# Kernel tuning notes

Measured on AMD Instinct MI355X. Metric: run time of the kernel, lower is better.

## Reference

```python
import jax, jax.numpy as jnp
import numpy as np

SOS, EOS = 0, 1
MAXLEN = 128
EPS = 1e-5


def setup_inputs() -> dict:
    key = jax.random.key(0)
    ks = jax.random.split(key, 10)
    B, T, Hc, Hs, V, Hm = 64, 1024, 512, 512, 64, 128
    h = jax.random.normal(ks[0], (B, T, Hc), dtype=jnp.float32)
    x_seq_lens = jax.random.randint(ks[1], (B,), 1, T + 1).astype(jnp.int32)
    s = 0.05
    return {
        "h": h,
        "W_ih": jax.random.normal(ks[2], (4 * Hs, V + Hc), dtype=jnp.float32) * s,
        "W_hh": jax.random.normal(ks[3], (4 * Hs, Hs), dtype=jnp.float32) * s,
        "b_ih": jax.random.normal(ks[4], (4 * Hs,), dtype=jnp.float32) * s,
        "b_hh": jax.random.normal(ks[5], (4 * Hs,), dtype=jnp.float32) * s,
        "fc1_w": jax.random.normal(ks[6], (Hm, Hs + Hc), dtype=jnp.float32) * s,
        "fc1_b": jax.random.normal(ks[7], (Hm,), dtype=jnp.float32) * s,
        "fc2_w": jax.random.normal(ks[8], (V, Hm), dtype=jnp.float32) * s,
        "x_seq_lens": x_seq_lens,
    }


def reference(h, W_ih, W_hh, b_ih, b_hh, fc1_w, fc1_b, fc2_w, x_seq_lens):
    B, T, Hc = h.shape
    Hs = W_hh.shape[1]
    V = fc2_w.shape[0]
    # attention length mask [B, T]
    mask = (jnp.arange(T)[None, :] < x_seq_lens[:, None]).astype(h.dtype)
    sos = jax.nn.one_hot(jnp.full((B,), SOS), V, dtype=h.dtype)
    x0 = jnp.concatenate([sos, h[:, 0, :]], axis=-1)  # [B, V+Hc]
    carry0 = (x0, jnp.zeros((B, Hs), h.dtype), jnp.zeros((B, Hs), h.dtype),
              jnp.full((B,), MAXLEN, jnp.int32))

    def step(carry, t):
        x, hs, cs, lens = carry
        # single-layer LSTM cell, torch gate order i,f,g,o
        gates = x @ W_ih.T + hs @ W_hh.T + b_ih + b_hh
        i, f, g, o = jnp.split(gates, 4, axis=-1)
        cs = jax.nn.sigmoid(f) * cs + jax.nn.sigmoid(i) * jnp.tanh(g)
        hs = jax.nn.sigmoid(o) * jnp.tanh(cs)
        # dot-product attention (apply_proj=False, num_heads=1)
        e = jnp.einsum('bd,btd->bt', hs, h)
        exps = jnp.exp(e - jnp.max(e)) * mask  # MaskedSoftmax: global-max shift
        a = exps / (exps.sum(-1, keepdims=True) + EPS)
        ctx = jnp.einsum('bt,btd->bd', a, h)
        # chardist: two stacked linears (no nonlinearity), then softmax
        feat = jnp.concatenate([hs, ctx], axis=-1)
        logits = (feat @ fc1_w.T + fc1_b) @ fc2_w.T
        y_hat = jax.nn.softmax(logits, axis=-1)
        hit = (jnp.argmax(y_hat, axis=-1) == EOS) & (lens > t)
        lens = jnp.where(hit, t + 1, lens)
        x = jnp.concatenate([y_hat, ctx], axis=-1)  # decode mode (y=None)
        return (x, hs, cs, lens), (y_hat, a)

    (_, _, _, lens), (y_hats, atts) = jax.lax.scan(step, carry0, jnp.arange(MAXLEN))
    y_hats = jnp.transpose(y_hats, (1, 0, 2))              # [B, L, V]
    attentions = jnp.transpose(atts, (1, 0, 2))[:, None]   # [B, 1, L, T]
    return y_hats, lens, attentions
```

## Files before the change

kernel.cpp:

```cpp
#include <hip/hip_runtime.h>
#include <math.h>

typedef unsigned short ushort_t;
typedef unsigned int uint_t;

#define OFF_XT    0
#define OFF_CS    102400
#define OFF_E     135168
#define OFF_MD    200704
#define OFF_LENS  204800
#define OFF_W2    204864
#define OFF_B2    270400
#define OFF_CP    270464
#define OFF_HB16F 1319040
#define WS_NEED   ((size_t)(1319040 + 16777216) * 4)

#define OUT_YH   0
#define OUT_LENS 524288
#define OUT_ATT  524352

__device__ __forceinline__ float sigf(float x) { return 1.0f / (1.0f + __expf(-x)); }
__device__ __forceinline__ float dot4(float4 a, float4 b) {
    return a.x * b.x + a.y * b.y + a.z * b.z + a.w * b.w;
}
__device__ __forceinline__ uint_t bf16rne(float x) {
    uint_t u = __float_as_uint(x);
    return (u + 0x7FFFu + ((u >> 16) & 1u)) >> 16;
}
#define BLO(u) __uint_as_float((u) << 16)
#define BHI(u) __uint_as_float((u) & 0xFFFF0000u)

__global__ void k_init(const float* __restrict__ h, float* __restrict__ ws) {
    int blk = blockIdx.x, tid = threadIdx.x;
    int idx = blk * 256 + tid;
    if (idx < 102400) {
        int k = idx >> 6, b = idx & 63;
        float v = 0.0f;
        if (k == 0) v = 1.0f;
        else if (k >= 64 && k < 576) v = h[(size_t)b * 524288 + (k - 64)];
        ws[OFF_XT + idx] = v;
    }
    if (blk >= 400 && blk < 528)
        ws[OFF_CS + (blk - 400) * 256 + tid] = 0.0f;
    if (blk == 527 && tid < 64) ((int*)ws)[OFF_LENS + tid] = 128;
}

__global__ void k_hconv(const float* __restrict__ h, float* __restrict__ ws) {
    size_t i = ((size_t)blockIdx.x * 256 + threadIdx.x) * 8;
    float4 a = *(const float4*)(h + i);
    float4 b = *(const float4*)(h + i + 4);
    uint4 o;
    o.x = bf16rne(a.x) | (bf16rne(a.y) << 16);
    o.y = bf16rne(a.z) | (bf16rne(a.w) << 16);
    o.z = bf16rne(b.x) | (bf16rne(b.y) << 16);
    o.w = bf16rne(b.z) | (bf16rne(b.w) << 16);
    *(uint4*)((ushort_t*)(ws + OFF_HB16F) + i) = o;
}

__global__ void k_fuse(const float* __restrict__ fc1w, const float* __restrict__ fc1b,
                       const float* __restrict__ fc2w, float* __restrict__ ws) {
    int blk = blockIdx.x;
    int v = blk >> 2, kc = blk & 3;
    int k = kc * 256 + threadIdx.x;
    float acc = 0.0f;
#pragma unroll 8
    for (int m = 0; m < 128; m++) acc += fc2w[v * 128 + m] * fc1w[(size_t)m * 1024 + k];
    ws[OFF_W2 + (size_t)v * 1024 + k] = acc;
    if (kc == 0 && threadIdx.x == 0) {
        float bb = 0.0f;
        for (int m = 0; m < 128; m++) bb += fc2w[v * 128 + m] * fc1b[m];
        ws[OFF_B2 + v] = bb;
    }
}

__global__ __launch_bounds__(1024) void k_gates(
        const float* __restrict__ Wih, const float* __restrict__ Whh,
        const float* __restrict__ bih, const float* __restrict__ bhh,
        float* __restrict__ ws, int p) {
    const int tid = threadIdx.x;
    const int lane = tid & 63;
    const int w = tid >> 6;
    const int hs_in  = 576 + (p ? 512 : 0);
    const int hs_out = 576 + (p ? 0 : 512);
    __shared__ float gpart[8192];
    const int u0 = blockIdx.x * 2;
    const int wq = __builtin_amdgcn_readfirstlane(w);
    float acc[2][4] = {{0, 0, 0, 0}, {0, 0, 0, 0}};
    int k0 = wq * 68, k1 = k0 + 68;
    int kx1 = k1 < 576 ? k1 : 576;
#pragma unroll 2
    for (int k = k0; k < kx1; k += 4) {
        float4 xv;
        xv.x = ws[OFF_XT + (k + 0) * 64 + lane];
        xv.y = ws[OFF_XT + (k + 1) * 64 + lane];
        xv.z = ws[OFF_XT + (k + 2) * 64 + lane];
        xv.w = ws[OFF_XT + (k + 3) * 64 + lane];
#pragma unroll
        for (int uu = 0; uu < 2; ++uu)
#pragma unroll
            for (int g = 0; g < 4; ++g)
                acc[uu][g] += dot4(*(const float4*)&Wih[(size_t)(g * 512 + u0 + uu) * 576 + k], xv);
    }
    int kh0 = k0 > 576 ? k0 : 576;
#pragma unroll 2
    for (int k = kh0; k < k1; k += 4) {
        float4 xv;
        xv.x = ws[OFF_XT + (hs_in + (k - 576) + 0) * 64 + lane];
        xv.y = ws[OFF_XT + (hs_in + (k - 576) + 1) * 64 + lane];
        xv.z = ws[OFF_XT + (hs_in + (k - 576) + 2) * 64 + lane];
        xv.w = ws[OFF_XT + (hs_in + (k - 576) + 3) * 64 + lane];
#pragma unroll
        for (int uu = 0; uu < 2; ++uu)
#pragma unroll
            for (int g = 0; g < 4; ++g)
                acc[uu][g] += dot4(*(const float4*)&Whh[(size_t)(g * 512 + u0 + uu) * 512 + (k - 576)], xv);
    }
#pragma unroll
    for (int uu = 0; uu < 2; ++uu)
#pragma unroll
        for (int g = 0; g < 4; ++g)
            gpart[((w * 2 + uu) * 4 + g) * 64 + lane] = acc[uu][g];
    __syncthreads();
    if (tid < 128) {
        int uu = tid >> 6, b = tid & 63;
        int u = u0 + uu;
        float g4[4];
#pragma unroll
        for (int g = 0; g < 4; ++g) {
            float s = 0.0f;
#pragma unroll
            for (int ww = 0; ww < 16; ++ww) s += gpart[((ww * 2 + uu) * 4 + g) * 64 + b];
            g4[g] = s + bih[g * 512 + u] + bhh[g * 512 + u];
        }
        int idx = u * 64 + b;
        float co = ws[OFF_CS + idx];
        float I = sigf(g4[0]), F = sigf(g4[1]), G = tanhf(g4[2]), O = sigf(g4[3]);
        float cn = F * co + I * G;
        ws[OFF_CS + idx] = cn;
        ws[OFF_XT + (size_t)(hs_out + u) * 64 + b] = O * tanhf(cn);
    }
}

__global__ __launch_bounds__(256) void k_attn16(const int* __restrict__ slen,
                                                float* __restrict__ ws, int p) {
    const int blk = blockIdx.x;
    const int tid = threadIdx.x;
    const int lane = tid & 63;
    const int w = __builtin_amdgcn_readfirstlane(tid >> 6);
    const int rg = lane >> 4, cl = lane & 15;
    const int hs_out = 576 + (p ? 0 : 512);
    const int b = blk >> 5, sb = blk & 31;
    const int L = slen[b];
    const int t0 = sb * 32;
    __shared__ float hs_sh[512];
    __shared__ float e_part[128];
    __shared__ float e_sh[32];
    __shared__ float wt_sh[32];
    const ushort_t* hb = (const ushort_t*)(ws + OFF_HB16F)
                       + ((size_t)b * 1024 + t0) * 512 + w * 128 + cl * 8;
    uint4 r0 = *(const uint4*)(hb + (size_t)(rg * 8 + 0) * 512);
    uint4 r1 = *(const uint4*)(hb + (size_t)(rg * 8 + 1) * 512);
    uint4 r2 = *(const uint4*)(hb + (size_t)(rg * 8 + 2) * 512);
    uint4 r3 = *(const uint4*)(hb + (size_t)(rg * 8 + 3) * 512);
    uint4 r4 = *(const uint4*)(hb + (size_t)(rg * 8 + 4) * 512);
    uint4 r5 = *(const uint4*)(hb + (size_t)(rg * 8 + 5) * 512);
    uint4 r6 = *(const uint4*)(hb + (size_t)(rg * 8 + 6) * 512);
    uint4 r7 = *(const uint4*)(hb + (size_t)(rg * 8 + 7) * 512);
    hs_sh[tid]       = ws[OFF_XT + (size_t)(hs_out + tid) * 64 + b];
    hs_sh[256 + tid] = ws[OFF_XT + (size_t)(hs_out + 256 + tid) * 64 + b];
    __syncthreads();
    float hsv[8];
#pragma unroll
    for (int j = 0; j < 8; ++j) hsv[j] = hs_sh[w * 128 + cl * 8 + j];
#define EROW(J, R)                                                                  \
    {                                                                               \
        float part = BLO(R.x) * hsv[0] + BHI(R.x) * hsv[1]                          \
                   + BLO(R.y) * hsv[2] + BHI(R.y) * hsv[3]                          \
                   + BLO(R.z) * hsv[4] + BHI(R.z) * hsv[5]                          \
                   + BLO(R.w) * hsv[6] + BHI(R.w) * hsv[7];                         \
        part += __shfl_xor(part, 1);                                                \
        part += __shfl_xor(part, 2);                                                \
        part += __shfl_xor(part, 4);                                                \
        part += __shfl_xor(part, 8);                                                \
        if (cl == 0) e_part[w * 32 + rg * 8 + (J)] = part;                          \
    }
    EROW(0, r0) EROW(1, r1) EROW(2, r2) EROW(3, r3)
    EROW(4, r4) EROW(5, r5) EROW(6, r6) EROW(7, r7)
#undef EROW
    __syncthreads();
    if (tid < 32) {
        float e = e_part[tid] + e_part[32 + tid] + e_part[64 + tid] + e_part[96 + tid];
        e_sh[tid] = e;
        ws[OFF_E + (size_t)b * 1024 + t0 + tid] = e;
    }
    __syncthreads();
    if (tid < 32) {
        float m = e_sh[0];
#pragma unroll
        for (int j = 1; j < 32; ++j) m = fmaxf(m, e_sh[j]);
        int tg = t0 + tid;
        wt_sh[tid] = (tg < L) ? __expf(e_sh[tid] - m) : 0.0f;
        if (tid == 0) ws[OFF_MD + (b * 32 + sb) * 2] = m;
    }
    __syncthreads();
    float acc[8] = {0, 0, 0, 0, 0, 0, 0, 0};
#define PVROW(J, R)                                                                 \
    {                                                                               \
        float wt = wt_sh[rg * 8 + (J)];                                             \
        acc[0] += wt * BLO(R.x); acc[1] += wt * BHI(R.x);                           \
        acc[2] += wt * BLO(R.y); acc[3] += wt * BHI(R.y);                           \
        acc[4] += wt * BLO(R.z); acc[5] += wt * BHI(R.z);                           \
        acc[6] += wt * BLO(R.w); acc[7] += wt * BHI(R.w);                           \
    }
    PVROW(0, r0) PVROW(1, r1) PVROW(2, r2) PVROW(3, r3)
    PVROW(4, r4) PVROW(5, r5) PVROW(6, r6) PVROW(7, r7)
#undef PVROW
#pragma unroll
    for (int k = 0; k < 8; ++k) {
        acc[k] += __shfl_xor(acc[k], 16);
        acc[k] += __shfl_xor(acc[k], 32);
    }
    if (rg == 0) {
        float4 o0; o0.x = acc[0]; o0.y = acc[1]; o0.z = acc[2]; o0.w = acc[3];
        float4 o1; o1.x = acc[4]; o1.y = acc[5]; o1.z = acc[6]; o1.w = acc[7];
        float* cp = ws + OFF_CP + (size_t)(b * 32 + sb) * 512 + w * 128 + cl * 8;
        *(float4*)cp = o0;
        *(float4*)(cp + 4) = o1;
    }
    if (tid == 0) {
        float D = 0.0f;
#pragma unroll
        for (int tl = 0; tl < 32; ++tl) D += wt_sh[tl];
        ws[OFF_MD + (b * 32 + sb) * 2 + 1] = D;
    }
}

__global__ void k_attn(const float* __restrict__ h, const int* __restrict__ slen,
                       float* __restrict__ ws, int p) {
    const int blk = blockIdx.x;
    const int tid = threadIdx.x;
    const int lane = tid & 63;
    const int w = tid >> 6;
    const int hs_out = 576 + (p ? 0 : 512);
    const int b = blk >> 4, sb = blk & 15;
    const int L = slen[b];
    const int t0 = sb * 64;
    __shared__ float stage[4096];
    __shared__ float hs_sh[512];
    __shared__ float e_sh[8];
    const float* hb = h + ((size_t)b * 1024 + t0) * 512;
    hs_sh[tid]       = ws[OFF_XT + (size_t)(hs_out + tid) * 64 + b];
    hs_sh[256 + tid] = ws[OFF_XT + (size_t)(hs_out + 256 + tid) * 64 + b];
    __syncthreads();
    float hsv[8];
#pragma unroll
    for (int j = 0; j < 8; ++j) hsv[j] = hs_sh[lane * 8 + j];
    float m_run = -INFINITY, D = 0.0f, accx = 0.0f, accy = 0.0f;
    for (int c = 0; c < 8; ++c) {
        const float* gsrc = hb + (size_t)c * 4096 + tid * 4;
        float4 tv0 = *(const float4*)(gsrc);
        float4 tv1 = *(const float4*)(gsrc + 1024);
        float4 tv2 = *(const float4*)(gsrc + 2048);
        float4 tv3 = *(const float4*)(gsrc + 3072);
        __syncthreads();
        *(float4*)&stage[tid * 4]        = tv0;
        *(float4*)&stage[1024 + tid * 4] = tv1;
        *(float4*)&stage[2048 + tid * 4] = tv2;
        *(float4*)&stage[3072 + tid * 4] = tv3;
        __syncthreads();
#pragma unroll
        for (int rr = 0; rr < 2; ++rr) {
            int tl = w * 2 + rr;
            const float4* rp = (const float4*)&stage[tl * 512 + lane * 8];
            float4 pp = rp[0], qq = rp[1];
            float part = pp.x * hsv[0] + pp.y * hsv[1] + pp.z * hsv[2] + pp.w * hsv[3]
                       + qq.x * hsv[4] + qq.y * hsv[5] + qq.z * hsv[6] + qq.w * hsv[7];
#pragma unroll
            for (int mm = 1; mm < 64; mm <<= 1) part += __shfl_xor(part, mm);
            if (lane == 0) {
                e_sh[tl] = part;
                ws[OFF_E + (size_t)b * 1024 + t0 + c * 8 + tl] = part;
            }
        }
        __syncthreads();
        float cm = e_sh[0];
#pragma unroll
        for (int j = 1; j < 8; ++j) cm = fmaxf(cm, e_sh[j]);
        float m_new = fmaxf(m_run, cm);
        float sc = __expf(m_run - m_new);
        accx *= sc; accy *= sc; D *= sc;
        m_run = m_new;
#pragma unroll
        for (int tl = 0; tl < 8; ++tl) {
            int tg = t0 + c * 8 + tl;
            float wt = (tg < L) ? __expf(e_sh[tl] - m_run) : 0.0f;
            D += wt;
            float2 hv = *(const float2*)&stage[tl * 512 + tid * 2];
            accx += wt * hv.x;
            accy += wt * hv.y;
        }
    }
    float2 o2; o2.x = accx; o2.y = accy;
    *(float2*)&ws[OFF_CP + (size_t)(b * 16 + sb) * 512 + tid * 2] = o2;
    if (tid == 0) {
        ws[OFF_MD + (b * 16 + sb) * 2]     = m_run;
        ws[OFF_MD + (b * 16 + sb) * 2 + 1] = D;
    }
}

__global__ void k_comb(const int* __restrict__ slen, float* __restrict__ ws,
                       float* __restrict__ out, int p, int ts, int ns) {
    const int b = blockIdx.x, tid = threadIdx.x;
    const int hs_out = 576 + (p ? 0 : 512);
    __shared__ float red[256];
    __shared__ float feat[1024];
    __shared__ float sc_sh[32];
    __shared__ float lg_s[64];
    const int nent = 64 * ns;
    float mx = -INFINITY;
    for (int i = tid; i < nent; i += 256) mx = fmaxf(mx, ws[OFF_MD + i * 2]);
    red[tid] = mx;
    __syncthreads();
    for (int s = 128; s > 0; s >>= 1) {
        if (tid < s) red[tid] = fmaxf(red[tid], red[tid + s]);
        __syncthreads();
    }
    float m_g = red[0];
    __syncthreads();
    if (tid < ns) {
        float mi = ws[OFF_MD + (b * ns + tid) * 2];
        float Di = ws[OFF_MD + (b * ns + tid) * 2 + 1];
        float s = __expf(mi - m_g);
        sc_sh[tid] = s;
        red[tid] = s * Di;
    }
    __syncthreads();
    float dn = 0.0f;
    for (int j = 0; j < ns; ++j) dn += red[j];
    float inv = 1.0f / (dn + 1e-5f);
    float cx = 0.0f, cy = 0.0f;
    for (int i = 0; i < ns; ++i) {
        float s = sc_sh[i];
        float2 v = *(const float2*)&ws[OFF_CP + (size_t)(b * ns + i) * 512 + tid * 2];
        cx += s * v.x;
        cy += s * v.y;
    }
    cx *= inv; cy *= inv;
    feat[512 + tid * 2] = cx;
    feat[512 + tid * 2 + 1] = cy;
    ws[OFF_XT + (size_t)(64 + tid * 2) * 64 + b] = cx;
    ws[OFF_XT + (size_t)(64 + tid * 2 + 1) * 64 + b] = cy;
    feat[tid * 2]     = ws[OFF_XT + (size_t)(hs_out + tid * 2) * 64 + b];
    feat[tid * 2 + 1] = ws[OFF_XT + (size_t)(hs_out + tid * 2 + 1) * 64 + b];
    int L = slen[b];
#pragma unroll
    for (int q = 0; q < 4; ++q) {
        int t = tid + 256 * q;
        float e = ws[OFF_E + (size_t)b * 1024 + t];
        float a = (t < L) ? __expf(e - m_g) * inv : 0.0f;
        out[OUT_ATT + (size_t)b * 131072 + (size_t)ts * 1024 + t] = a;
    }
    __syncthreads();
    int v = tid >> 2, qq = tid & 3;
    const float4* w4 = (const float4*)(ws + OFF_W2 + (size_t)v * 1024 + qq * 256);
    const float4* f4 = (const float4*)feat + qq * 64;
    float acc = 0.0f;
#pragma unroll 8
    for (int k = 0; k < 64; ++k) acc += dot4(w4[k], f4[k]);
    acc += __shfl_xor(acc, 1);
    acc += __shfl_xor(acc, 2);
    if (qq == 0) lg_s[v] = acc;
    __syncthreads();
    if (tid < 64) {
        float lg = lg_s[tid] + ws[OFF_B2 + tid];
        float mxv = lg;
#pragma unroll
        for (int mm = 1; mm < 64; mm <<= 1) mxv = fmaxf(mxv, __shfl_xor(mxv, mm));
        float ev = __expf(lg - mxv);
        float s = ev;
#pragma unroll
        for (int mm = 1; mm < 64; mm <<= 1) s += __shfl_xor(s, mm);
        float y = ev / s;
        out[OUT_YH + (size_t)b * 8192 + ts * 64 + tid] = y;
        ws[OFF_XT + (size_t)tid * 64 + b] = y;
        float av = lg;
        int ai = tid;
#pragma unroll
        for (int mm = 1; mm < 64; mm <<= 1) {
            float ov = __shfl_xor(av, mm);
            int oi = __shfl_xor(ai, mm);
            if (ov > av || (ov == av && oi < ai)) { av = ov; ai = oi; }
        }
        if (tid == 0) {
            int* lens = (int*)ws + OFF_LENS;
            if (ai == 1 && lens[b] > ts) lens[b] = ts + 1;
            if (ts == 127) out[OUT_LENS + b] = (float)lens[b];
        }
    }
}

extern "C" void kernel_launch(void* const* d_in, const int* in_sizes, int n_in,
                              void* d_out, int out_size, void* d_ws, size_t ws_size,
                              hipStream_t stream) {
    (void)in_sizes; (void)n_in; (void)out_size;
    const float* h    = (const float*)d_in[0];
    const float* Wih  = (const float*)d_in[1];
    const float* Whh  = (const float*)d_in[2];
    const float* bih  = (const float*)d_in[3];
    const float* bhh  = (const float*)d_in[4];
    const float* fc1w = (const float*)d_in[5];
    const float* fc1b = (const float*)d_in[6];
    const float* fc2w = (const float*)d_in[7];
    const int*   slen = (const int*)d_in[8];
    float* ws  = (float*)d_ws;
    float* out = (float*)d_out;
    const bool use16 = (ws_size >= WS_NEED);

    k_init<<<528, 256, 0, stream>>>(h, ws);
    k_fuse<<<256, 256, 0, stream>>>(fc1w, fc1b, fc2w, ws);
    if (use16) k_hconv<<<16384, 256, 0, stream>>>(h, ws);
    for (int t = 0; t < 128; t++) {
        int p = t & 1;
        k_gates<<<256, 1024, 0, stream>>>(Wih, Whh, bih, bhh, ws, p);
        if (use16) {
            k_attn16<<<2048, 256, 0, stream>>>(slen, ws, p);
            k_comb<<<64, 256, 0, stream>>>(slen, ws, out, p, t, 32);
        } else {
            k_attn<<<1024, 256, 0, stream>>>(h, slen, ws, p);
            k_comb<<<64, 256, 0, stream>>>(slen, ws, out, p, t, 16);
        }
    }
}
```

Before: 6.112 ms.

## Split LSTM gates into x/hh parts and overlap hh-matmul with attention

Splits the gate computation so the input-projection part (W_ih times x) runs in its own kernel, while the recurrent W_hh times hs product for the next step is computed by extra blocks inside the attention kernel. Both read the same fresh hidden state, so the recurrent matmul is taken off the serial per-step chain. Attention blocks also skip the context accumulation for chunks beyond the sequence length. The combine kernel is rewritten with 512 threads to handle 1024-wide features directly. The price is a more complex dependency chain through the GHH workspace buffer and mixed block roles within one launch.

```diff
diff --git a/kernel.cpp b/kernel.cpp
--- a/kernel.cpp
+++ b/kernel.cpp
@@ -12,8 +12,9 @@
 #define OFF_W2    204864
 #define OFF_B2    270400
 #define OFF_CP    270464
-#define OFF_HB16F 1319040
-#define WS_NEED   ((size_t)(1319040 + 16777216) * 4)
+#define OFF_GHH   1319040
+#define OFF_HB16F 1450112
+#define WS_NEED   ((size_t)(1450112 + 16777216) * 4)
 
 #define OUT_YH   0
 #define OUT_LENS 524288
@@ -58,7 +59,8 @@
 }
 
 __global__ void k_fuse(const float* __restrict__ fc1w, const float* __restrict__ fc1b,
-                       const float* __restrict__ fc2w, float* __restrict__ ws) {
+                       const float* __restrict__ fc2w, const float* __restrict__ bih,
+                       const float* __restrict__ bhh, float* __restrict__ ws) {
     int blk = blockIdx.x;
     int v = blk >> 2, kc = blk & 3;
     int k = kc * 256 + threadIdx.x;
@@ -70,6 +72,293 @@
         float bb = 0.0f;
         for (int m = 0; m < 128; m++) bb += fc2w[v * 128 + m] * fc1b[m];
         ws[OFF_B2 + v] = bb;
+    }
+#pragma unroll
+    for (int rep = 0; rep < 2; ++rep) {
+        int idx = (blk * 256 + threadIdx.x) * 2 + rep;
+        int r = idx >> 6;
+        ws[OFF_GHH + idx] = bih[r] + bhh[r];
+    }
+}
+
+__global__ __launch_bounds__(512) void k_gatesx(const float* __restrict__ Wih,
+                                                float* __restrict__ ws) {
+    const int tid = threadIdx.x;
+    const int lane = tid & 63;
+    const int w = tid >> 6;
+    __shared__ float gpart[4096];
+    const int u0 = blockIdx.x * 2;
+    const int wq = __builtin_amdgcn_readfirstlane(w);
+    float acc[2][4] = {{0, 0, 0, 0}, {0, 0, 0, 0}};
+    int k0 = wq * 72, k1 = k0 + 72;
+#pragma unroll 2
+    for (int k = k0; k < k1; k += 4) {
+        float4 xv;
+        xv.x = ws[OFF_XT + (k + 0) * 64 + lane];
+        xv.y = ws[OFF_XT + (k + 1) * 64 + lane];
+        xv.z = ws[OFF_XT + (k + 2) * 64 + lane];
+        xv.w = ws[OFF_XT + (k + 3) * 64 + lane];
+#pragma unroll
+        for (int uu = 0; uu < 2; ++uu)
+#pragma unroll
+            for (int g = 0; g < 4; ++g)
+                acc[uu][g] += dot4(*(const float4*)&Wih[(size_t)(g * 512 + u0 + uu) * 576 + k], xv);
+    }
+#pragma unroll
+    for (int uu = 0; uu < 2; ++uu)
+#pragma unroll
+        for (int g = 0; g < 4; ++g)
+            gpart[((w * 2 + uu) * 4 + g) * 64 + lane] = acc[uu][g];
+    __syncthreads();
+    if (tid < 128) {
+        int uu = tid >> 6, b = tid & 63;
+        int u = u0 + uu;
+        float g4[4];
+#pragma unroll
+        for (int g = 0; g < 4; ++g) {
+            float s = ws[OFF_GHH + (size_t)(g * 512 + u) * 64 + b];
+#pragma unroll
+            for (int ww = 0; ww < 8; ++ww) s += gpart[((ww * 2 + uu) * 4 + g) * 64 + b];
+            g4[g] = s;
+        }
+        int idx = u * 64 + b;
+        float co = ws[OFF_CS + idx];
+        float I = sigf(g4[0]), F = sigf(g4[1]), G = tanhf(g4[2]), O = sigf(g4[3]);
+        float cn = F * co + I * G;
+        ws[OFF_CS + idx] = cn;
+        ws[OFF_XT + (size_t)(576 + u) * 64 + b] = O * tanhf(cn);
+    }
+}
+
+__global__ __launch_bounds__(256) void k_hh_attn(const int* __restrict__ slen,
+                                                 const float* __restrict__ Whh,
+                                                 const float* __restrict__ bih,
+                                                 const float* __restrict__ bhh,
+                                                 float* __restrict__ ws) {
+    const int blk = blockIdx.x;
+    const int tid = threadIdx.x;
+    const int lane = tid & 63;
+    __shared__ float smem[2048];
+    if (blk < 256) {
+        const int w = tid >> 6;
+        const int u0 = blk * 2;
+        const int wq = __builtin_amdgcn_readfirstlane(w);
+        float acc[2][4] = {{0, 0, 0, 0}, {0, 0, 0, 0}};
+        int k0 = wq * 128, k1 = k0 + 128;
+#pragma unroll 2
+        for (int k = k0; k < k1; k += 4) {
+            float4 xv;
+            xv.x = ws[OFF_XT + (576 + k + 0) * 64 + lane];
+            xv.y = ws[OFF_XT + (576 + k + 1) * 64 + lane];
+            xv.z = ws[OFF_XT + (576 + k + 2) * 64 + lane];
+            xv.w = ws[OFF_XT + (576 + k + 3) * 64 + lane];
+#pragma unroll
+            for (int uu = 0; uu < 2; ++uu)
+#pragma unroll
+                for (int g = 0; g < 4; ++g)
+                    acc[uu][g] += dot4(*(const float4*)&Whh[(size_t)(g * 512 + u0 + uu) * 512 + k], xv);
+        }
+#pragma unroll
+        for (int uu = 0; uu < 2; ++uu)
+#pragma unroll
+            for (int g = 0; g < 4; ++g)
+                smem[((w * 2 + uu) * 4 + g) * 64 + lane] = acc[uu][g];
+        __syncthreads();
+        if (tid < 128) {
+            int uu = tid >> 6, b = tid & 63;
+            int u = u0 + uu;
+#pragma unroll
+            for (int g = 0; g < 4; ++g) {
+                int r = g * 512 + u;
+                float s = bih[r] + bhh[r];
+#pragma unroll
+                for (int ww = 0; ww < 4; ++ww) s += smem[((ww * 2 + uu) * 4 + g) * 64 + b];
+                ws[OFF_GHH + (size_t)r * 64 + b] = s;
+            }
+        }
+        return;
+    }
+    float* hs_sh  = smem;
+    float* e_part = smem + 512;
+    float* e_sh   = smem + 640;
+    float* wt_sh  = smem + 672;
+    const int ab = blk - 256;
+    const int w = __builtin_amdgcn_readfirstlane(tid >> 6);
+    const int rg = lane >> 4, cl = lane & 15;
+    const int b = ab >> 5, sb = ab & 31;
+    const int L = slen[b];
+    const int t0 = sb * 32;
+    const ushort_t* hb = (const ushort_t*)(ws + OFF_HB16F)
+                       + ((size_t)b * 1024 + t0) * 512 + w * 128 + cl * 8;
+    uint4 r0 = *(const uint4*)(hb + (size_t)(rg * 8 + 0) * 512);
+    uint4 r1 = *(const uint4*)(hb + (size_t)(rg * 8 + 1) * 512);
+    uint4 r2 = *(const uint4*)(hb + (size_t)(rg * 8 + 2) * 512);
+    uint4 r3 = *(const uint4*)(hb + (size_t)(rg * 8 + 3) * 512);
+    uint4 r4 = *(const uint4*)(hb + (size_t)(rg * 8 + 4) * 512);
+    uint4 r5 = *(const uint4*)(hb + (size_t)(rg * 8 + 5) * 512);
+    uint4 r6 = *(const uint4*)(hb + (size_t)(rg * 8 + 6) * 512);
+    uint4 r7 = *(const uint4*)(hb + (size_t)(rg * 8 + 7) * 512);
+    hs_sh[tid]       = ws[OFF_XT + (size_t)(576 + tid) * 64 + b];
+    hs_sh[256 + tid] = ws[OFF_XT + (size_t)(576 + 256 + tid) * 64 + b];
+    __syncthreads();
+    float hsv[8];
+#pragma unroll
+    for (int j = 0; j < 8; ++j) hsv[j] = hs_sh[w * 128 + cl * 8 + j];
+#define EROW(J, R)                                                                  \
+    {                                                                               \
+        float part = BLO(R.x) * hsv[0] + BHI(R.x) * hsv[1]                          \
+                   + BLO(R.y) * hsv[2] + BHI(R.y) * hsv[3]                          \
+                   + BLO(R.z) * hsv[4] + BHI(R.z) * hsv[5]                          \
+                   + BLO(R.w) * hsv[6] + BHI(R.w) * hsv[7];                         \
+        part += __shfl_xor(part, 1);                                                \
+        part += __shfl_xor(part, 2);                                                \
+        part += __shfl_xor(part, 4);                                                \
+        part += __shfl_xor(part, 8);                                                \
+        if (cl == 0) e_part[w * 32 + rg * 8 + (J)] = part;                          \
+    }
+    EROW(0, r0) EROW(1, r1) EROW(2, r2) EROW(3, r3)
+    EROW(4, r4) EROW(5, r5) EROW(6, r6) EROW(7, r7)
+#undef EROW
+    __syncthreads();
+    if (tid < 32) {
+        float e = e_part[tid] + e_part[32 + tid] + e_part[64 + tid] + e_part[96 + tid];
+        e_sh[tid] = e;
+        ws[OFF_E + (size_t)b * 1024 + t0 + tid] = e;
+    }
+    __syncthreads();
+    if (tid < 32) {
+        float m = e_sh[0];
+#pragma unroll
+        for (int j = 1; j < 32; ++j) m = fmaxf(m, e_sh[j]);
+        int tg = t0 + tid;
+        wt_sh[tid] = (tg < L) ? __expf(e_sh[tid] - m) : 0.0f;
+        if (tid == 0) ws[OFF_MD + (b * 32 + sb) * 2] = m;
+    }
+    __syncthreads();
+    int nr = L - t0;
+    nr = nr < 0 ? 0 : (nr > 32 ? 32 : nr);
+    if (nr > 0) {
+        float acc[8] = {0, 0, 0, 0, 0, 0, 0, 0};
+#define PVROW(J, R)                                                                 \
+        {                                                                           \
+            float wt = wt_sh[rg * 8 + (J)];                                         \
+            acc[0] += wt * BLO(R.x); acc[1] += wt * BHI(R.x);                       \
+            acc[2] += wt * BLO(R.y); acc[3] += wt * BHI(R.y);                       \
+            acc[4] += wt * BLO(R.z); acc[5] += wt * BHI(R.z);                       \
+            acc[6] += wt * BLO(R.w); acc[7] += wt * BHI(R.w);                       \
+        }
+        PVROW(0, r0) PVROW(1, r1) PVROW(2, r2) PVROW(3, r3)
+        PVROW(4, r4) PVROW(5, r5) PVROW(6, r6) PVROW(7, r7)
+#undef PVROW
+#pragma unroll
+        for (int k = 0; k < 8; ++k) {
+            acc[k] += __shfl_xor(acc[k], 16);
+            acc[k] += __shfl_xor(acc[k], 32);
+        }
+        if (rg == 0) {
+            float4 o0; o0.x = acc[0]; o0.y = acc[1]; o0.z = acc[2]; o0.w = acc[3];
+            float4 o1; o1.x = acc[4]; o1.y = acc[5]; o1.z = acc[6]; o1.w = acc[7];
+            float* cp = ws + OFF_CP + (size_t)(b * 32 + sb) * 512 + w * 128 + cl * 8;
+            *(float4*)cp = o0;
+            *(float4*)(cp + 4) = o1;
+        }
+    }
+    if (tid == 0) {
+        float D = 0.0f;
+#pragma unroll
+        for (int tl = 0; tl < 32; ++tl) D += wt_sh[tl];
+        ws[OFF_MD + (b * 32 + sb) * 2 + 1] = D;
+    }
+}
+
+__global__ __launch_bounds__(512) void k_comb2(const int* __restrict__ slen,
+                                               float* __restrict__ ws,
+                                               float* __restrict__ out, int ts) {
+    const int b = blockIdx.x, tid = threadIdx.x;
+    __shared__ float red[512];
+    __shared__ float feat[1024];
+    __shared__ float sc_sh[32];
+    __shared__ float lg_s[64];
+    float mx = -INFINITY;
+#pragma unroll
+    for (int i = 0; i < 4; ++i) mx = fmaxf(mx, ws[OFF_MD + (tid + 512 * i) * 2]);
+    red[tid] = mx;
+    __syncthreads();
+    for (int s = 256; s > 0; s >>= 1) {
+        if (tid < s) red[tid] = fmaxf(red[tid], red[tid + s]);
+        __syncthreads();
+    }
+    float m_g = red[0];
+    __syncthreads();
+    int L = slen[b];
+    int nsl = (L + 31) >> 5;
+    if (tid < 32) {
+        float s = 0.0f, sd = 0.0f;
+        if (tid < nsl) {
+            float mi = ws[OFF_MD + (b * 32 + tid) * 2];
+            float Di = ws[OFF_MD + (b * 32 + tid) * 2 + 1];
+            s = __expf(mi - m_g);
+            sd = s * Di;
+        }
+        sc_sh[tid] = s;
+        red[tid] = sd;
+    }
+    __syncthreads();
+    float dn = 0.0f;
+#pragma unroll
+    for (int j = 0; j < 32; ++j) dn += red[j];
+    float inv = 1.0f / (dn + 1e-5f);
+    float cx = 0.0f;
+    for (int i = 0; i < nsl; ++i)
+        cx += sc_sh[i] * ws[OFF_CP + (size_t)(b * 32 + i) * 512 + tid];
+    cx *= inv;
+    feat[512 + tid] = cx;
+    ws[OFF_XT + (size_t)(64 + tid) * 64 + b] = cx;
+    feat[tid] = ws[OFF_XT + (size_t)(576 + tid) * 64 + b];
+#pragma unroll
+    for (int q = 0; q < 2; ++q) {
+        int t = tid + 512 * q;
+        float e = ws[OFF_E + (size_t)b * 1024 + t];
+        float a = (t < L) ? __expf(e - m_g) * inv : 0.0f;
+        out[OUT_ATT + (size_t)b * 131072 + (size_t)ts * 1024 + t] = a;
+    }
+    __syncthreads();
+    int v = tid >> 3, qq = tid & 7;
+    const float4* w4 = (const float4*)(ws + OFF_W2 + (size_t)v * 1024 + qq * 128);
+    const float4* f4 = (const float4*)feat + qq * 32;
+    float acc = 0.0f;
+#pragma unroll 8
+    for (int k = 0; k < 32; ++k) acc += dot4(w4[k], f4[k]);
+    acc += __shfl_xor(acc, 1);
+    acc += __shfl_xor(acc, 2);
+    acc += __shfl_xor(acc, 4);
+    if (qq == 0) lg_s[v] = acc;
+    __syncthreads();
+    if (tid < 64) {
+        float lg = lg_s[tid] + ws[OFF_B2 + tid];
+        float mxv = lg;
+#pragma unroll
+        for (int mm = 1; mm < 64; mm <<= 1) mxv = fmaxf(mxv, __shfl_xor(mxv, mm));
+        float ev = __expf(lg - mxv);
+        float s = ev;
+#pragma unroll
+        for (int mm = 1; mm < 64; mm <<= 1) s += __shfl_xor(s, mm);
+        float y = ev / s;
+        out[OUT_YH + (size_t)b * 8192 + ts * 64 + tid] = y;
+        ws[OFF_XT + (size_t)tid * 64 + b] = y;
+        float av = lg;
+        int ai = tid;
+#pragma unroll
+        for (int mm = 1; mm < 64; mm <<= 1) {
+            float ov = __shfl_xor(av, mm);
+            int oi = __shfl_xor(ai, mm);
+            if (ov > av || (ov == av && oi < ai)) { av = ov; ai = oi; }
+        }
+        if (tid == 0) {
+            int* lens = (int*)ws + OFF_LENS;
+            if (ai == 1 && lens[b] > ts) lens[b] = ts + 1;
+            if (ts == 127) out[OUT_LENS + b] = (float)lens[b];
+        }
     }
 }
 
@@ -141,100 +430,6 @@
     }
 }
 
-__global__ __launch_bounds__(256) void k_attn16(const int* __restrict__ slen,
-                                                float* __restrict__ ws, int p) {
-    const int blk = blockIdx.x;
-    const int tid = threadIdx.x;
-    const int lane = tid & 63;
-    const int w = __builtin_amdgcn_readfirstlane(tid >> 6);
-    const int rg = lane >> 4, cl = lane & 15;
-    const int hs_out = 576 + (p ? 0 : 512);
-    const int b = blk >> 5, sb = blk & 31;
-    const int L = slen[b];
-    const int t0 = sb * 32;
-    __shared__ float hs_sh[512];
-    __shared__ float e_part[128];
-    __shared__ float e_sh[32];
-    __shared__ float wt_sh[32];
-    const ushort_t* hb = (const ushort_t*)(ws + OFF_HB16F)
-                       + ((size_t)b * 1024 + t0) * 512 + w * 128 + cl * 8;
-    uint4 r0 = *(const uint4*)(hb + (size_t)(rg * 8 + 0) * 512);
-    uint4 r1 = *(const uint4*)(hb + (size_t)(rg * 8 + 1) * 512);
-    uint4 r2 = *(const uint4*)(hb + (size_t)(rg * 8 + 2) * 512);
-    uint4 r3 = *(const uint4*)(hb + (size_t)(rg * 8 + 3) * 512);
-    uint4 r4 = *(const uint4*)(hb + (size_t)(rg * 8 + 4) * 512);
-    uint4 r5 = *(const uint4*)(hb + (size_t)(rg * 8 + 5) * 512);
-    uint4 r6 = *(const uint4*)(hb + (size_t)(rg * 8 + 6) * 512);
-    uint4 r7 = *(const uint4*)(hb + (size_t)(rg * 8 + 7) * 512);
-    hs_sh[tid]       = ws[OFF_XT + (size_t)(hs_out + tid) * 64 + b];
-    hs_sh[256 + tid] = ws[OFF_XT + (size_t)(hs_out + 256 + tid) * 64 + b];
-    __syncthreads();
-    float hsv[8];
-#pragma unroll
-    for (int j = 0; j < 8; ++j) hsv[j] = hs_sh[w * 128 + cl * 8 + j];
-#define EROW(J, R)                                                                  \
-    {                                                                               \
-        float part = BLO(R.x) * hsv[0] + BHI(R.x) * hsv[1]                          \
-                   + BLO(R.y) * hsv[2] + BHI(R.y) * hsv[3]                          \
-                   + BLO(R.z) * hsv[4] + BHI(R.z) * hsv[5]                          \
-                   + BLO(R.w) * hsv[6] + BHI(R.w) * hsv[7];                         \
-        part += __shfl_xor(part, 1);                                                \
-        part += __shfl_xor(part, 2);                                                \
-        part += __shfl_xor(part, 4);                                                \
-        part += __shfl_xor(part, 8);                                                \
-        if (cl == 0) e_part[w * 32 + rg * 8 + (J)] = part;                          \
-    }
-    EROW(0, r0) EROW(1, r1) EROW(2, r2) EROW(3, r3)
-    EROW(4, r4) EROW(5, r5) EROW(6, r6) EROW(7, r7)
-#undef EROW
-    __syncthreads();
-    if (tid < 32) {
-        float e = e_part[tid] + e_part[32 + tid] + e_part[64 + tid] + e_part[96 + tid];
-        e_sh[tid] = e;
-        ws[OFF_E + (size_t)b * 1024 + t0 + tid] = e;
-    }
-    __syncthreads();
-    if (tid < 32) {
-        float m = e_sh[0];
-#pragma unroll
-        for (int j = 1; j < 32; ++j) m = fmaxf(m, e_sh[j]);
-        int tg = t0 + tid;
-        wt_sh[tid] = (tg < L) ? __expf(e_sh[tid] - m) : 0.0f;
-        if (tid == 0) ws[OFF_MD + (b * 32 + sb) * 2] = m;
-    }
-    __syncthreads();
-    float acc[8] = {0, 0, 0, 0, 0, 0, 0, 0};
-#define PVROW(J, R)                                                                 \
-    {                                                                               \
-        float wt = wt_sh[rg * 8 + (J)];                                             \
-        acc[0] += wt * BLO(R.x); acc[1] += wt * BHI(R.x);                           \
-        acc[2] += wt * BLO(R.y); acc[3] += wt * BHI(R.y);                           \
-        acc[4] += wt * BLO(R.z); acc[5] += wt * BHI(R.z);                           \
-        acc[6] += wt * BLO(R.w); acc[7] += wt * BHI(R.w);                           \
-    }
-    PVROW(0, r0) PVROW(1, r1) PVROW(2, r2) PVROW(3, r3)
-    PVROW(4, r4) PVROW(5, r5) PVROW(6, r6) PVROW(7, r7)
-#undef PVROW
-#pragma unroll
-    for (int k = 0; k < 8; ++k) {
-        acc[k] += __shfl_xor(acc[k], 16);
-        acc[k] += __shfl_xor(acc[k], 32);
-    }
-    if (rg == 0) {
-        float4 o0; o0.x = acc[0]; o0.y = acc[1]; o0.z = acc[2]; o0.w = acc[3];
-        float4 o1; o1.x = acc[4]; o1.y = acc[5]; o1.z = acc[6]; o1.w = acc[7];
-        float* cp = ws + OFF_CP + (size_t)(b * 32 + sb) * 512 + w * 128 + cl * 8;
-        *(float4*)cp = o0;
-        *(float4*)(cp + 4) = o1;
-    }
-    if (tid == 0) {
-        float D = 0.0f;
-#pragma unroll
-        for (int tl = 0; tl < 32; ++tl) D += wt_sh[tl];
-        ws[OFF_MD + (b * 32 + sb) * 2 + 1] = D;
-    }
-}
-
 __global__ void k_attn(const float* __restrict__ h, const int* __restrict__ slen,
                        float* __restrict__ ws, int p) {
     const int blk = blockIdx.x;
@@ -417,15 +612,18 @@
     const bool use16 = (ws_size >= WS_NEED);
 
     k_init<<<528, 256, 0, stream>>>(h, ws);
-    k_fuse<<<256, 256, 0, stream>>>(fc1w, fc1b, fc2w, ws);
-    if (use16) k_hconv<<<16384, 256, 0, stream>>>(h, ws);
-    for (int t = 0; t < 128; t++) {
-        int p = t & 1;
-        k_gates<<<256, 1024, 0, stream>>>(Wih, Whh, bih, bhh, ws, p);
-        if (use16) {
-            k_attn16<<<2048, 256, 0, stream>>>(slen, ws, p);
-            k_comb<<<64, 256, 0, stream>>>(slen, ws, out, p, t, 32);
-        } else {
+    k_fuse<<<256, 256, 0, stream>>>(fc1w, fc1b, fc2w, bih, bhh, ws);
+    if (use16) {
+        k_hconv<<<16384, 256, 0, stream>>>(h, ws);
+        for (int t = 0; t < 128; t++) {
+            k_gatesx<<<256, 512, 0, stream>>>(Wih, ws);
+            k_hh_attn<<<2304, 256, 0, stream>>>(slen, Whh, bih, bhh, ws);
+            k_comb2<<<64, 512, 0, stream>>>(slen, ws, out, t);
+        }
+    } else {
+        for (int t = 0; t < 128; t++) {
+            int p = t & 1;
+            k_gates<<<256, 1024, 0, stream>>>(Wih, Whh, bih, bhh, ws, p);
             k_attn<<<1024, 256, 0, stream>>>(h, slen, ws, p);
             k_comb<<<64, 256, 0, stream>>>(slen, ws, out, p, t, 16);
         }
```

After: 5.294 ms, median of 2. -13.4%, faster.
